# Kernel tuning notes

Hardware: AMD Instinct MI355X
Metric: run time of the kernel (lower is better)

The kernel has to match this reference:

```python
import jax, jax.numpy as jnp
import numpy as np

E, H, F, T, K = 32, 1024, 512, 1024, 8

def setup_inputs() -> dict:
    key = jax.random.key(0)
    k1, k2, k3, k4, k5 = jax.random.split(key, 5)
    return {
        "hidden_states": jax.random.normal(k1, (T, H), dtype=jnp.float32),
        "top_k_index": jax.random.randint(k2, (T, K), 0, E),
        "top_k_weights": jax.random.uniform(k3, (T, K), dtype=jnp.float32),
        "gate_up_proj": jax.random.normal(k4, (E, 2 * F, H), dtype=jnp.float32),
        "down_proj": jax.random.normal(k5, (E, H, F), dtype=jnp.float32),
    }

def reference(hidden_states, top_k_index, top_k_weights, gate_up_proj, down_proj):
    n_experts = gate_up_proj.shape[0]
    T_ = hidden_states.shape[0]
    # Combine routing weights into dense [T, E] map (duplicates accumulate,
    # matching torch's index_add_ semantics).
    w = jnp.zeros((T_, n_experts), dtype=hidden_states.dtype)
    w = w.at[jnp.arange(T_)[:, None], top_k_index].add(top_k_weights)
    ffn = down_proj.shape[-1]

    def step(final, params):
        Wgu, Wd, we = params  # [2F,H], [H,F], [T]
        gu = hidden_states @ Wgu.T            # [T, 2F]
        gate, up = gu[:, :ffn], gu[:, ffn:]
        out = (jax.nn.silu(gate) * up) @ Wd.T  # [T, H]
        return final + we[:, None] * out, None

    final, _ = jax.lax.scan(step, jnp.zeros_like(hidden_states),
                            (gate_up_proj, down_proj, w.T))
    return final
```

## Files before the change

kernel.cpp:

```cpp
#include <hip/hip_runtime.h>
#include <hip/hip_bf16.h>

#define NE     32
#define HD     1024
#define FF     512
#define NT     1024
#define TOPK   8
#define NPAIR  (NT * TOPK)
#define MAXT2  96

typedef __attribute__((ext_vector_type(8))) short  bf16x8;
typedef __attribute__((ext_vector_type(4))) float  f32x4;

__device__ __forceinline__ unsigned short f2bf_rne(float f) {
    unsigned u = __float_as_uint(f);
    u += 0x7FFFu + ((u >> 16) & 1u);
    return (unsigned short)(u >> 16);
}

__device__ __forceinline__ unsigned pk2(float x, float y) {
    __hip_bfloat162 h = __float22bfloat162_rn(float2{x, y});
    union { __hip_bfloat162 h; unsigned u; } c;
    c.h = h;
    return c.u;
}

__device__ __forceinline__ uint4 pk8(const float* __restrict__ p) {
    float4 a = *(const float4*)p;
    float4 b = *(const float4*)(p + 4);
    uint4 r;
    r.x = pk2(a.x, a.y);
    r.y = pk2(a.z, a.w);
    r.z = pk2(b.x, b.y);
    r.w = pk2(b.z, b.w);
    return r;
}


__global__ __launch_bounds__(1024) void k_route(const int* __restrict__ idx,
                                                const float* __restrict__ tkw,
                                                int* __restrict__ meta) {
    __shared__ int sc[NE], scur[NE], soff[NE + 1];
    __shared__ int ste[MAXT2], stm[MAXT2], snt;
    int tid = threadIdx.x;
    if (tid < NE) { sc[tid] = 0; scur[tid] = 0; }
    __syncthreads();
    int e8[TOPK];
#pragma unroll
    for (int j = 0; j < TOPK; j++) { e8[j] = idx[tid * TOPK + j]; atomicAdd(&sc[e8[j]], 1); }
    __syncthreads();
    if (tid == 0) {
        int off = 0, nt = 0;
        for (int e = 0; e < NE; e++) {
            soff[e] = off;
            for (int s = 0; s < sc[e]; s += 128) { ste[nt] = e; stm[nt] = s; nt++; }
            off += sc[e];
        }
        soff[NE] = off; snt = nt;
    }
    __syncthreads();
    int*   tok_list = meta + 256;
    float* w_list   = (float*)(meta + 8448);
    int*   posmap   = meta + 16640;
#pragma unroll
    for (int j = 0; j < TOPK; j++) {
        int e = e8[j];
        int p = soff[e] + atomicAdd(&scur[e], 1);
        tok_list[p] = tid;
        w_list[p]   = tkw[tid * TOPK + j];
        posmap[tid * TOPK + j] = p;
    }
    if (tid <= NE) meta[1 + tid] = soff[tid];
    if (tid == 0)  meta[0] = snt;
    if (tid < MAXT2) { meta[64 + tid] = (tid < snt) ? ste[tid] : 0;
                       meta[160 + tid] = (tid < snt) ? stm[tid] : 0; }
}

__global__ __launch_bounds__(256) void k_mm1(
        const float* __restrict__ hs, const float* __restrict__ wgu,
        const int* __restrict__ meta, unsigned short* __restrict__ A) {
    int numt = meta[0];
    int bx = blockIdx.x;
    if (bx >= numt) return;
    int e   = meta[64 + bx], m0 = meta[160 + bx];
    int seg = meta[1 + e];
    int nrows = meta[1 + e + 1] - seg - m0;
    if (nrows > 128) nrows = 128;
    int c0 = blockIdx.y * 64;
    const int* tok_list = meta + 256;
    const float* w_list = (const float*)(meta + 8448);

    __shared__ __align__(16) unsigned short Xs[128][40];
    __shared__ __align__(16) unsigned short Ws[128][40];
    __shared__ int   toks[128];
    __shared__ float wrow[128];
    int tid = threadIdx.x;
    if (tid < 128) {
        toks[tid] = (tid < nrows) ? tok_list[seg + m0 + tid] : -1;
        wrow[tid] = (tid < nrows) ? w_list[seg + m0 + tid] : 0.f;
    }
    __syncthreads();

    int wave = tid >> 6, lane = tid & 63, lr = lane & 15, lk = lane >> 4;
    f32x4 accg[2][4] = {}, accu[2][4] = {};
    const float* wbase = wgu + (size_t)e * 2 * FF * HD;

    for (int k0 = 0; k0 < HD; k0 += 32) {
        for (int c = tid; c < 512; c += 256) {
            int r = c >> 2, cc = c & 3;
            int tk = toks[r];
            uint4 xv = make_uint4(0, 0, 0, 0);
            if (tk >= 0) xv = pk8(hs + (size_t)tk * HD + k0 + cc * 8);
            *(uint4*)&Xs[r][cc * 8] = xv;
            int grow = (r < 64) ? (c0 + r) : (FF + c0 + (r - 64));
            *(uint4*)&Ws[r][cc * 8] = pk8(wbase + (size_t)grow * HD + k0 + cc * 8);
        }
        __syncthreads();
        bf16x8 a0 = *(const bf16x8*)&Xs[wave * 32 + lr][lk * 8];
        bf16x8 a1 = *(const bf16x8*)&Xs[wave * 32 + 16 + lr][lk * 8];
#pragma unroll
        for (int cf = 0; cf < 4; cf++) {
            bf16x8 bg = *(const bf16x8*)&Ws[cf * 16 + lr][lk * 8];
            bf16x8 bu = *(const bf16x8*)&Ws[64 + cf * 16 + lr][lk * 8];
            accg[0][cf] = __builtin_amdgcn_mfma_f32_16x16x32_bf16(a0, bg, accg[0][cf], 0, 0, 0);
            accg[1][cf] = __builtin_amdgcn_mfma_f32_16x16x32_bf16(a1, bg, accg[1][cf], 0, 0, 0);
            accu[0][cf] = __builtin_amdgcn_mfma_f32_16x16x32_bf16(a0, bu, accu[0][cf], 0, 0, 0);
            accu[1][cf] = __builtin_amdgcn_mfma_f32_16x16x32_bf16(a1, bu, accu[1][cf], 0, 0, 0);
        }
        __syncthreads();
    }
#pragma unroll
    for (int rf = 0; rf < 2; rf++)
#pragma unroll
        for (int q = 0; q < 4; q++) {
            int r = wave * 32 + rf * 16 + lk * 4 + q;
            if (r < nrows) {
                float w = wrow[r];
#pragma unroll
                for (int cf = 0; cf < 4; cf++) {
                    float g = accg[rf][cf][q], u = accu[rf][cf][q];
                    float act = (g / (1.f + __expf(-g))) * u * w;
                    A[(size_t)(seg + m0 + r) * FF + c0 + cf * 16 + lr] = f2bf_rne(act);
                }
            }
        }
}

__global__ __launch_bounds__(256) void k_mm2(
        const unsigned short* __restrict__ A, const float* __restrict__ wd,
        const int* __restrict__ meta, float* __restrict__ O) {
    int numt = meta[0];
    int bx = blockIdx.x;
    if (bx >= numt) return;
    int e   = meta[64 + bx], m0 = meta[160 + bx];
    int seg = meta[1 + e];
    int nrows = meta[1 + e + 1] - seg - m0;
    if (nrows > 128) nrows = 128;
    int n0 = blockIdx.y * 128;

    __shared__ __align__(16) unsigned short Xs[128][40];
    __shared__ __align__(16) unsigned short Ws[128][40];
    int tid = threadIdx.x;
    int wave = tid >> 6, lane = tid & 63, lr = lane & 15, lk = lane >> 4;
    f32x4 acc[2][8] = {};
    const float* wbase = wd + (size_t)e * HD * FF;

    for (int k0 = 0; k0 < FF; k0 += 32) {
        for (int c = tid; c < 512; c += 256) {
            int r = c >> 2, cc = c & 3;
            uint4 xv = make_uint4(0, 0, 0, 0);
            if (r < nrows) xv = *(const uint4*)(A + (size_t)(seg + m0 + r) * FF + k0 + cc * 8);
            *(uint4*)&Xs[r][cc * 8] = xv;
            *(uint4*)&Ws[r][cc * 8] = pk8(wbase + (size_t)(n0 + r) * FF + k0 + cc * 8);
        }
        __syncthreads();
        bf16x8 a0 = *(const bf16x8*)&Xs[wave * 32 + lr][lk * 8];
        bf16x8 a1 = *(const bf16x8*)&Xs[wave * 32 + 16 + lr][lk * 8];
#pragma unroll
        for (int cf = 0; cf < 8; cf++) {
            bf16x8 b = *(const bf16x8*)&Ws[cf * 16 + lr][lk * 8];
            acc[0][cf] = __builtin_amdgcn_mfma_f32_16x16x32_bf16(a0, b, acc[0][cf], 0, 0, 0);
            acc[1][cf] = __builtin_amdgcn_mfma_f32_16x16x32_bf16(a1, b, acc[1][cf], 0, 0, 0);
        }
        __syncthreads();
    }
#pragma unroll
    for (int rf = 0; rf < 2; rf++)
#pragma unroll
        for (int q = 0; q < 4; q++) {
            int r = wave * 32 + rf * 16 + lk * 4 + q;
            if (r < nrows) {
#pragma unroll
                for (int cf = 0; cf < 8; cf++)
                    O[(size_t)(seg + m0 + r) * HD + n0 + cf * 16 + lr] = acc[rf][cf][q];
            }
        }
}

__global__ void k_reduce(const float* __restrict__ O, const int* __restrict__ posmap,
                         float* __restrict__ out) {
    int i = blockIdx.x * blockDim.x + threadIdx.x;
    int t = i >> 8, c4 = i & 255;
    float4 acc = make_float4(0.f, 0.f, 0.f, 0.f);
#pragma unroll
    for (int k = 0; k < TOPK; k++) {
        int p = posmap[t * TOPK + k];
        float4 v = ((const float4*)(O + (size_t)p * HD))[c4];
        acc.x += v.x; acc.y += v.y; acc.z += v.z; acc.w += v.w;
    }
    ((float4*)out)[i] = acc;
}

extern "C" void kernel_launch(void* const* d_in, const int* in_sizes, int n_in,
                              void* d_out, int out_size, void* d_ws, size_t ws_size,
                              hipStream_t stream) {
    const float* hs  = (const float*)d_in[0];
    const int*   idx = (const int*)  d_in[1];
    const float* tkw = (const float*)d_in[2];
    const float* wgu = (const float*)d_in[3];
    const float* wd  = (const float*)d_in[4];
    float* out = (float*)d_out;

    const size_t OFF_A = 128 * 1024;
    const size_t OFF_O = OFF_A + (size_t)NPAIR * FF * 2;

    char* ws = (char*)d_ws;
    int* meta = (int*)ws;
    unsigned short* A_bf = (unsigned short*)(ws + OFF_A);
    float* O_rows        = (float*)(ws + OFF_O);
    const int* posmap    = meta + 16640;

    k_route<<<1, 1024, 0, stream>>>(idx, tkw, meta);
    dim3 g1(MAXT2, FF / 64);
    k_mm1<<<g1, 256, 0, stream>>>(hs, wgu, meta, A_bf);
    dim3 g2(MAXT2, HD / 128);
    k_mm2<<<g2, 256, 0, stream>>>(A_bf, wd, meta, O_rows);
    k_reduce<<<NT * HD / 4 / 256, 256, 0, stream>>>(O_rows, posmap, out);
}
```

Measured before the change: 133.6 us.

## Pre-convert weights to bf16, async LDS-pipelined MoE matmuls with atomic scatter

Adds kernels that convert all expert weights to bf16 and gather routed token rows into a bf16 buffer each call. Both matmuls then stream tiles with global_load_lds into a triple-buffered, XOR-swizzled LDS pipeline with a block-index swizzle. The down projection scatters results with float atomics into a zeroed output, which replaces the separate reduction kernel. The cost is an extra full pass over fp32 weights each call, plus atomic contention and nondeterministic summation.

```diff
diff --git a/kernel.cpp b/kernel.cpp
--- a/kernel.cpp
+++ b/kernel.cpp
@@ -17,25 +17,36 @@
     u += 0x7FFFu + ((u >> 16) & 1u);
     return (unsigned short)(u >> 16);
 }
-
 __device__ __forceinline__ unsigned pk2(float x, float y) {
     __hip_bfloat162 h = __float22bfloat162_rn(float2{x, y});
     union { __hip_bfloat162 h; unsigned u; } c;
     c.h = h;
     return c.u;
 }
-
-__device__ __forceinline__ uint4 pk8(const float* __restrict__ p) {
-    float4 a = *(const float4*)p;
-    float4 b = *(const float4*)(p + 4);
+__device__ __forceinline__ uint4 pk8q(float4 a, float4 b) {
     uint4 r;
-    r.x = pk2(a.x, a.y);
-    r.y = pk2(a.z, a.w);
-    r.z = pk2(b.x, b.y);
-    r.w = pk2(b.z, b.w);
+    r.x = pk2(a.x, a.y); r.y = pk2(a.z, a.w);
+    r.z = pk2(b.x, b.y); r.w = pk2(b.z, b.w);
     return r;
 }
-
+__device__ __forceinline__ void gload16(const void* g, void* l) {
+    __builtin_amdgcn_global_load_lds(
+        (const __attribute__((address_space(1))) unsigned int*)g,
+        (__attribute__((address_space(3))) unsigned int*)l, 16, 0, 0);
+}
+#define MFMA16(a, b, c) __builtin_amdgcn_mfma_f32_16x16x32_bf16(a, b, c, 0, 0, 0)
+
+#define PIPE_SYNC(LAST) do {                                       \
+    if (LAST) asm volatile("s_waitcnt vmcnt(0)" ::: "memory");     \
+    else      asm volatile("s_waitcnt vmcnt(4)" ::: "memory");     \
+    __builtin_amdgcn_s_barrier();                                  \
+    __builtin_amdgcn_sched_barrier(0);                             \
+} while (0)
+
+#define OFF_XG (128u * 1024u)
+#define OFF_AB (OFF_XG + 8320u * 2048u)
+#define OFF_WG (OFF_AB + 8320u * 1024u)
+#define OFF_WD (OFF_WG + 67108864u)
 
 __global__ __launch_bounds__(1024) void k_route(const int* __restrict__ idx,
                                                 const float* __restrict__ tkw,
@@ -76,58 +87,111 @@
                        meta[160 + tid] = (tid < snt) ? stm[tid] : 0; }
 }
 
+__global__ void k_gather(const float* __restrict__ hs, const int* __restrict__ meta,
+                         unsigned short* __restrict__ Xg) {
+    int i = blockIdx.x * blockDim.x + threadIdx.x;
+    int p = i >> 7, c = (i & 127) << 3;
+    int tok = meta[256 + p];
+    float4 a = *(const float4*)(hs + (size_t)tok * HD + c);
+    float4 b = *(const float4*)(hs + (size_t)tok * HD + c + 4);
+    *(uint4*)(Xg + (size_t)p * HD + c) = pk8q(a, b);
+}
+
+__global__ void k_cvtw(const float* __restrict__ wgu, const float* __restrict__ wd,
+                       unsigned short* __restrict__ wgu_bf, unsigned short* __restrict__ wd_bf) {
+    const int GU8 = NE * 2 * FF * HD / 8;
+    const int TOT = GU8 + NE * HD * FF / 8;
+    int stride = gridDim.x * blockDim.x;
+    for (int c = blockIdx.x * blockDim.x + threadIdx.x; c < TOT; c += stride) {
+        const float* s; unsigned short* d; int j;
+        if (c < GU8) { s = wgu; d = wgu_bf; j = c; }
+        else         { s = wd;  d = wd_bf;  j = c - GU8; }
+        float4 a = ((const float4*)s)[j * 2];
+        float4 b = ((const float4*)s)[j * 2 + 1];
+        ((uint4*)d)[j] = pk8q(a, b);
+    }
+}
+
+__global__ void k_zero(float* __restrict__ out) {
+    int i = blockIdx.x * blockDim.x + threadIdx.x;
+    ((float4*)out)[i] = make_float4(0.f, 0.f, 0.f, 0.f);
+}
+
 __global__ __launch_bounds__(256) void k_mm1(
-        const float* __restrict__ hs, const float* __restrict__ wgu,
-        const int* __restrict__ meta, unsigned short* __restrict__ A) {
+        const unsigned short* __restrict__ Xg, const unsigned short* __restrict__ wgu_bf,
+        const int* __restrict__ meta, const float* __restrict__ w_list,
+        unsigned short* __restrict__ A) {
+    int lid = blockIdx.x;
+    int wsw = (lid & 7) * 96 + (lid >> 3);
+    int bx = wsw >> 3, by = wsw & 7;
     int numt = meta[0];
-    int bx = blockIdx.x;
     if (bx >= numt) return;
     int e   = meta[64 + bx], m0 = meta[160 + bx];
     int seg = meta[1 + e];
-    int nrows = meta[1 + e + 1] - seg - m0;
+    int nrows = meta[2 + e] - seg - m0;
     if (nrows > 128) nrows = 128;
-    int c0 = blockIdx.y * 64;
-    const int* tok_list = meta + 256;
-    const float* w_list = (const float*)(meta + 8448);
-
-    __shared__ __align__(16) unsigned short Xs[128][40];
-    __shared__ __align__(16) unsigned short Ws[128][40];
-    __shared__ int   toks[128];
-    __shared__ float wrow[128];
+    int c0 = by * 64;
+
+    __shared__ __align__(16) unsigned char Xb[3][8192];
+    __shared__ __align__(16) unsigned char Wb[3][8192];
     int tid = threadIdx.x;
-    if (tid < 128) {
-        toks[tid] = (tid < nrows) ? tok_list[seg + m0 + tid] : -1;
-        wrow[tid] = (tid < nrows) ? w_list[seg + m0 + tid] : 0.f;
-    }
-    __syncthreads();
-
     int wave = tid >> 6, lane = tid & 63, lr = lane & 15, lk = lane >> 4;
+
+    unsigned Lp0 = (unsigned)(wave * 2) * 1024u + (unsigned)lane * 16u;
+    unsigned Lp1 = Lp0 + 1024u;
+    unsigned xr0 = Lp0 >> 6, xr1 = Lp1 >> 6;
+    unsigned sc0 = (Lp0 & 63u) ^ (((Lp0 >> 7) & 3u) << 4);
+    unsigned sc1 = (Lp1 & 63u) ^ (((Lp1 >> 7) & 3u) << 4);
+    const unsigned char* xs0 = (const unsigned char*)Xg + (size_t)(seg + m0 + xr0) * (HD * 2) + sc0;
+    const unsigned char* xs1 = (const unsigned char*)Xg + (size_t)(seg + m0 + xr1) * (HD * 2) + sc1;
+    unsigned g0 = (xr0 < 64) ? (c0 + xr0) : (FF + c0 + (xr0 - 64));
+    unsigned g1 = (xr1 < 64) ? (c0 + xr1) : (FF + c0 + (xr1 - 64));
+    const unsigned char* ws0 = (const unsigned char*)wgu_bf + ((size_t)e * (2 * FF) + g0) * (HD * 2) + sc0;
+    const unsigned char* ws1 = (const unsigned char*)wgu_bf + ((size_t)e * (2 * FF) + g1) * (HD * 2) + sc1;
+
+    unsigned aoff[2], goff[4], uoff[4];
+#pragma unroll
+    for (int rf = 0; rf < 2; rf++) {
+        unsigned row = wave * 32 + rf * 16 + lr;
+        aoff[rf] = row * 64 + (((unsigned)lk * 16) ^ (((row >> 1) & 3u) << 4));
+    }
+#pragma unroll
+    for (int cf = 0; cf < 4; cf++) {
+        unsigned rg = cf * 16 + lr, ru = 64 + cf * 16 + lr;
+        goff[cf] = rg * 64 + (((unsigned)lk * 16) ^ (((rg >> 1) & 3u) << 4));
+        uoff[cf] = ru * 64 + (((unsigned)lk * 16) ^ (((ru >> 1) & 3u) << 4));
+    }
+
     f32x4 accg[2][4] = {}, accu[2][4] = {};
-    const float* wbase = wgu + (size_t)e * 2 * FF * HD;
-
-    for (int k0 = 0; k0 < HD; k0 += 32) {
-        for (int c = tid; c < 512; c += 256) {
-            int r = c >> 2, cc = c & 3;
-            int tk = toks[r];
-            uint4 xv = make_uint4(0, 0, 0, 0);
-            if (tk >= 0) xv = pk8(hs + (size_t)tk * HD + k0 + cc * 8);
-            *(uint4*)&Xs[r][cc * 8] = xv;
-            int grow = (r < 64) ? (c0 + r) : (FF + c0 + (r - 64));
-            *(uint4*)&Ws[r][cc * 8] = pk8(wbase + (size_t)grow * HD + k0 + cc * 8);
-        }
-        __syncthreads();
-        bf16x8 a0 = *(const bf16x8*)&Xs[wave * 32 + lr][lk * 8];
-        bf16x8 a1 = *(const bf16x8*)&Xs[wave * 32 + 16 + lr][lk * 8];
+#pragma unroll
+    for (int b = 0; b < 2; b++) {
+        gload16(xs0, &Xb[b][Lp0]); gload16(xs1, &Xb[b][Lp1]);
+        gload16(ws0, &Wb[b][Lp0]); gload16(ws1, &Wb[b][Lp1]);
+        xs0 += 64; xs1 += 64; ws0 += 64; ws1 += 64;
+    }
+
+    const int NSTEP = HD / 32;
+    for (int t = 0; t < NSTEP; ++t) {
+        PIPE_SYNC(t + 1 >= NSTEP);
+        if (t + 2 < NSTEP) {
+            int nb = (t + 2) % 3;
+            gload16(xs0, &Xb[nb][Lp0]); gload16(xs1, &Xb[nb][Lp1]);
+            gload16(ws0, &Wb[nb][Lp0]); gload16(ws1, &Wb[nb][Lp1]);
+            xs0 += 64; xs1 += 64; ws0 += 64; ws1 += 64;
+        }
+        const unsigned char* xb = Xb[t % 3];
+        const unsigned char* wb = Wb[t % 3];
+        bf16x8 af0 = *(const bf16x8*)(xb + aoff[0]);
+        bf16x8 af1 = *(const bf16x8*)(xb + aoff[1]);
 #pragma unroll
         for (int cf = 0; cf < 4; cf++) {
-            bf16x8 bg = *(const bf16x8*)&Ws[cf * 16 + lr][lk * 8];
-            bf16x8 bu = *(const bf16x8*)&Ws[64 + cf * 16 + lr][lk * 8];
-            accg[0][cf] = __builtin_amdgcn_mfma_f32_16x16x32_bf16(a0, bg, accg[0][cf], 0, 0, 0);
-            accg[1][cf] = __builtin_amdgcn_mfma_f32_16x16x32_bf16(a1, bg, accg[1][cf], 0, 0, 0);
-            accu[0][cf] = __builtin_amdgcn_mfma_f32_16x16x32_bf16(a0, bu, accu[0][cf], 0, 0, 0);
-            accu[1][cf] = __builtin_amdgcn_mfma_f32_16x16x32_bf16(a1, bu, accu[1][cf], 0, 0, 0);
-        }
-        __syncthreads();
+            bf16x8 bg = *(const bf16x8*)(wb + goff[cf]);
+            bf16x8 bu = *(const bf16x8*)(wb + uoff[cf]);
+            accg[0][cf] = MFMA16(af0, bg, accg[0][cf]);
+            accg[1][cf] = MFMA16(af1, bg, accg[1][cf]);
+            accu[0][cf] = MFMA16(af0, bu, accu[0][cf]);
+            accu[1][cf] = MFMA16(af1, bu, accu[1][cf]);
+        }
     }
 #pragma unroll
     for (int rf = 0; rf < 2; rf++)
@@ -135,7 +199,7 @@
         for (int q = 0; q < 4; q++) {
             int r = wave * 32 + rf * 16 + lk * 4 + q;
             if (r < nrows) {
-                float w = wrow[r];
+                float w = w_list[seg + m0 + r];
 #pragma unroll
                 for (int cf = 0; cf < 4; cf++) {
                     float g = accg[rf][cf][q], u = accu[rf][cf][q];
@@ -147,68 +211,87 @@
 }
 
 __global__ __launch_bounds__(256) void k_mm2(
-        const unsigned short* __restrict__ A, const float* __restrict__ wd,
-        const int* __restrict__ meta, float* __restrict__ O) {
+        const unsigned short* __restrict__ A, const unsigned short* __restrict__ wd_bf,
+        const int* __restrict__ meta, float* __restrict__ out) {
+    int lid = blockIdx.x;
+    int wsw = (lid & 7) * 96 + (lid >> 3);
+    int bx = wsw >> 3, by = wsw & 7;
     int numt = meta[0];
-    int bx = blockIdx.x;
     if (bx >= numt) return;
     int e   = meta[64 + bx], m0 = meta[160 + bx];
     int seg = meta[1 + e];
-    int nrows = meta[1 + e + 1] - seg - m0;
+    int nrows = meta[2 + e] - seg - m0;
     if (nrows > 128) nrows = 128;
-    int n0 = blockIdx.y * 128;
-
-    __shared__ __align__(16) unsigned short Xs[128][40];
-    __shared__ __align__(16) unsigned short Ws[128][40];
+    int n0 = by * 128;
+
+    __shared__ __align__(16) unsigned char Xb[3][8192];
+    __shared__ __align__(16) unsigned char Wb[3][8192];
     int tid = threadIdx.x;
     int wave = tid >> 6, lane = tid & 63, lr = lane & 15, lk = lane >> 4;
+
+    unsigned Lp0 = (unsigned)(wave * 2) * 1024u + (unsigned)lane * 16u;
+    unsigned Lp1 = Lp0 + 1024u;
+    unsigned xr0 = Lp0 >> 6, xr1 = Lp1 >> 6;
+    unsigned sc0 = (Lp0 & 63u) ^ (((Lp0 >> 7) & 3u) << 4);
+    unsigned sc1 = (Lp1 & 63u) ^ (((Lp1 >> 7) & 3u) << 4);
+    const unsigned char* xs0 = (const unsigned char*)A + (size_t)(seg + m0 + xr0) * (FF * 2) + sc0;
+    const unsigned char* xs1 = (const unsigned char*)A + (size_t)(seg + m0 + xr1) * (FF * 2) + sc1;
+    const unsigned char* ws0 = (const unsigned char*)wd_bf + ((size_t)e * HD + n0 + xr0) * (FF * 2) + sc0;
+    const unsigned char* ws1 = (const unsigned char*)wd_bf + ((size_t)e * HD + n0 + xr1) * (FF * 2) + sc1;
+
+    unsigned aoff[2], boff[8];
+#pragma unroll
+    for (int rf = 0; rf < 2; rf++) {
+        unsigned row = wave * 32 + rf * 16 + lr;
+        aoff[rf] = row * 64 + (((unsigned)lk * 16) ^ (((row >> 1) & 3u) << 4));
+    }
+#pragma unroll
+    for (int cf = 0; cf < 8; cf++) {
+        unsigned row = cf * 16 + lr;
+        boff[cf] = row * 64 + (((unsigned)lk * 16) ^ (((row >> 1) & 3u) << 4));
+    }
+
     f32x4 acc[2][8] = {};
-    const float* wbase = wd + (size_t)e * HD * FF;
-
-    for (int k0 = 0; k0 < FF; k0 += 32) {
-        for (int c = tid; c < 512; c += 256) {
-            int r = c >> 2, cc = c & 3;
-            uint4 xv = make_uint4(0, 0, 0, 0);
-            if (r < nrows) xv = *(const uint4*)(A + (size_t)(seg + m0 + r) * FF + k0 + cc * 8);
-            *(uint4*)&Xs[r][cc * 8] = xv;
-            *(uint4*)&Ws[r][cc * 8] = pk8(wbase + (size_t)(n0 + r) * FF + k0 + cc * 8);
-        }
-        __syncthreads();
-        bf16x8 a0 = *(const bf16x8*)&Xs[wave * 32 + lr][lk * 8];
-        bf16x8 a1 = *(const bf16x8*)&Xs[wave * 32 + 16 + lr][lk * 8];
+#pragma unroll
+    for (int b = 0; b < 2; b++) {
+        gload16(xs0, &Xb[b][Lp0]); gload16(xs1, &Xb[b][Lp1]);
+        gload16(ws0, &Wb[b][Lp0]); gload16(ws1, &Wb[b][Lp1]);
+        xs0 += 64; xs1 += 64; ws0 += 64; ws1 += 64;
+    }
+
+    const int NSTEP = FF / 32;
+    for (int t = 0; t < NSTEP; ++t) {
+        PIPE_SYNC(t + 1 >= NSTEP);
+        if (t + 2 < NSTEP) {
+            int nb = (t + 2) % 3;
+            gload16(xs0, &Xb[nb][Lp0]); gload16(xs1, &Xb[nb][Lp1]);
+            gload16(ws0, &Wb[nb][Lp0]); gload16(ws1, &Wb[nb][Lp1]);
+            xs0 += 64; xs1 += 64; ws0 += 64; ws1 += 64;
+        }
+        const unsigned char* xb = Xb[t % 3];
+        const unsigned char* wb = Wb[t % 3];
+        bf16x8 af0 = *(const bf16x8*)(xb + aoff[0]);
+        bf16x8 af1 = *(const bf16x8*)(xb + aoff[1]);
 #pragma unroll
         for (int cf = 0; cf < 8; cf++) {
-            bf16x8 b = *(const bf16x8*)&Ws[cf * 16 + lr][lk * 8];
-            acc[0][cf] = __builtin_amdgcn_mfma_f32_16x16x32_bf16(a0, b, acc[0][cf], 0, 0, 0);
-            acc[1][cf] = __builtin_amdgcn_mfma_f32_16x16x32_bf16(a1, b, acc[1][cf], 0, 0, 0);
-        }
-        __syncthreads();
-    }
+            bf16x8 b = *(const bf16x8*)(wb + boff[cf]);
+            acc[0][cf] = MFMA16(af0, b, acc[0][cf]);
+            acc[1][cf] = MFMA16(af1, b, acc[1][cf]);
+        }
+    }
+    const int* tok_list = meta + 256;
 #pragma unroll
     for (int rf = 0; rf < 2; rf++)
 #pragma unroll
         for (int q = 0; q < 4; q++) {
             int r = wave * 32 + rf * 16 + lk * 4 + q;
             if (r < nrows) {
+                int tok = tok_list[seg + m0 + r];
 #pragma unroll
                 for (int cf = 0; cf < 8; cf++)
-                    O[(size_t)(seg + m0 + r) * HD + n0 + cf * 16 + lr] = acc[rf][cf][q];
+                    atomicAdd(&out[(size_t)tok * HD + n0 + cf * 16 + lr], acc[rf][cf][q]);
             }
         }
-}
-
-__global__ void k_reduce(const float* __restrict__ O, const int* __restrict__ posmap,
-                         float* __restrict__ out) {
-    int i = blockIdx.x * blockDim.x + threadIdx.x;
-    int t = i >> 8, c4 = i & 255;
-    float4 acc = make_float4(0.f, 0.f, 0.f, 0.f);
-#pragma unroll
-    for (int k = 0; k < TOPK; k++) {
-        int p = posmap[t * TOPK + k];
-        float4 v = ((const float4*)(O + (size_t)p * HD))[c4];
-        acc.x += v.x; acc.y += v.y; acc.z += v.z; acc.w += v.w;
-    }
-    ((float4*)out)[i] = acc;
 }
 
 extern "C" void kernel_launch(void* const* d_in, const int* in_sizes, int n_in,
@@ -221,19 +304,18 @@
     const float* wd  = (const float*)d_in[4];
     float* out = (float*)d_out;
 
-    const size_t OFF_A = 128 * 1024;
-    const size_t OFF_O = OFF_A + (size_t)NPAIR * FF * 2;
-
     char* ws = (char*)d_ws;
     int* meta = (int*)ws;
-    unsigned short* A_bf = (unsigned short*)(ws + OFF_A);
-    float* O_rows        = (float*)(ws + OFF_O);
-    const int* posmap    = meta + 16640;
+    unsigned short* Xg     = (unsigned short*)(ws + OFF_XG);
+    unsigned short* A_bf   = (unsigned short*)(ws + OFF_AB);
+    unsigned short* wgu_bf = (unsigned short*)(ws + OFF_WG);
+    unsigned short* wd_bf  = (unsigned short*)(ws + OFF_WD);
+    const float* w_list    = (const float*)(meta + 8448);
 
     k_route<<<1, 1024, 0, stream>>>(idx, tkw, meta);
-    dim3 g1(MAXT2, FF / 64);
-    k_mm1<<<g1, 256, 0, stream>>>(hs, wgu, meta, A_bf);
-    dim3 g2(MAXT2, HD / 128);
-    k_mm2<<<g2, 256, 0, stream>>>(A_bf, wd, meta, O_rows);
-    k_reduce<<<NT * HD / 4 / 256, 256, 0, stream>>>(O_rows, posmap, out);
-}
+    k_cvtw<<<4096, 256, 0, stream>>>(wgu, wd, wgu_bf, wd_bf);
+    k_gather<<<NPAIR * (HD / 8) / 256, 256, 0, stream>>>(hs, meta, Xg);
+    k_zero<<<NT * HD / 4 / 256, 256, 0, stream>>>(out);
+    k_mm1<<<MAXT2 * 8, 256, 0, stream>>>(Xg, wgu_bf, meta, w_list, A_bf);
+    k_mm2<<<MAXT2 * 8, 256, 0, stream>>>(A_bf, wd_bf, meta, out);
+}
```

Measured after the change: 164.6 us. 23.2% more time.
